# Optimization experiments

Measured on AMD Instinct MI355X. Metric: run time of the kernel, lower is better.

Reference implementation:

```python
import jax, jax.numpy as jnp
import numpy as np

POS_IDX = np.array([0, 2, 4, 10, 14, 20, 22, 24])   # +w taps on 5x5 ring
NEG_IDX = np.array([6, 7, 8, 11, 13, 16, 17, 18])   # -w taps on inner 3x3 ring (center stays 0)


def setup_inputs() -> dict:
    key = jax.random.key(0)
    kx, kw = jax.random.split(key)
    x = jax.random.normal(kx, (16, 256, 128, 128), dtype=jnp.float32)
    weight = jax.random.normal(kw, (256, 1, 3, 3), dtype=jnp.float32) * 0.1
    return {"x": x, "weight": weight}


def _build_rpdc_kernel(weight):
    # weight: [C, 1, 3, 3] -> sparse 5x5 kernel [C, 1, 5, 5]
    C = weight.shape[0]
    w = weight.reshape(C, 1, 9)
    tap = w[:, :, 1:]  # taps 1..8 (skip w[0]); center of 5x5 is forced to 0
    buf = jnp.zeros((C, 1, 25), dtype=weight.dtype)
    buf = buf.at[:, :, POS_IDX].set(tap)
    buf = buf.at[:, :, NEG_IDX].set(-tap)
    return buf.reshape(C, 1, 5, 5)


def reference(x, weight):
    # Depthwise conv (groups = in_channels), dilation=1 -> padding = 2 (same conv)
    C = weight.shape[0]
    kernel = _build_rpdc_kernel(weight)
    return jax.lax.conv_general_dilated(
        x, kernel,
        window_strides=(1, 1),
        padding=[(2, 2), (2, 2)],
        rhs_dilation=(1, 1),
        dimension_numbers=("NCHW", "OIHW", "NCHW"),
        feature_group_count=C,
    )
```

## Files before the change

### kernel.cpp

```cpp
#include <hip/hip_runtime.h>


#define HH 128
#define WW 128
#define CHUNK 32
#define SPB 8

__device__ __forceinline__ float bperm(int addr, float v) {
    return __int_as_float(__builtin_amdgcn_ds_bpermute(addr, __float_as_int(v)));
}

__global__ __launch_bounds__(256, 4) void rpdc_kernel(
    const float* __restrict__ x, const float* __restrict__ wt,
    float* __restrict__ out, int C)
{
    const int tid   = threadIdx.x;
    const int l     = tid & 31;
    const int s     = blockIdx.x * SPB + (tid >> 5);
    const int plane = s >> 2;
    const int h0    = (s & 3) * CHUNK;
    const int c     = plane & (C - 1);

    const float* wp = wt + (size_t)c * 9;
    const float t0 = wp[1], t1 = wp[2], t2 = wp[3], t3 = wp[4];
    const float t4 = wp[5], t5 = wp[6], t6 = wp[7], t7 = wp[8];

    const int w0 = l * 4;
    const float ml = (l == 0) ? 0.f : 1.f;
    const float mr = (l == 31) ? 0.f : 1.f;

    const int lane = tid & 63;
    const int upA  = ((lane - 1) & 63) * 4;
    const int dnA  = ((lane + 1) & 63) * 4;

    const float* xb = x + (size_t)plane * (HH * WW) + (size_t)h0 * WW + w0;
    float* ob = out + (size_t)plane * (HH * WW) + (size_t)h0 * WW + w0;

    float ring[6][8];
    float4 s0, s1;

    auto issue = [&](int rr, float4& v) {
        const int r = h0 + rr;
        if ((unsigned)r < (unsigned)HH) {
            v = *(const float4*)(xb + rr * WW);
        } else {
            v = make_float4(0.f, 0.f, 0.f, 0.f);
        }
    };
    auto insert = [&](float (&row)[8], const float4& v) {
        row[0] = bperm(upA, v.z) * ml;
        row[1] = bperm(upA, v.w) * ml;
        row[2] = v.x; row[3] = v.y; row[4] = v.z; row[5] = v.w;
        row[6] = bperm(dnA, v.x) * mr;
        row[7] = bperm(dnA, v.y) * mr;
    };

#pragma unroll
    for (int k = 0; k < 5; ++k) {
        float4 v;
        issue(k - 2, v);
        insert(ring[k], v);
    }
    issue(3, s0);
    issue(4, s1);

#pragma unroll
    for (int h = 0; h < CHUNK; ++h) {
        float4 nv;
        issue((h <= CHUNK - 4) ? (h + 5) : HH, nv);

        insert(ring[(h + 5) % 6], s0);
        s0 = s1; s1 = nv;

        const float (&A)[8]  = ring[h % 6];
        const float (&B)[8]  = ring[(h + 1) % 6];
        const float (&Cc)[8] = ring[(h + 2) % 6];
        const float (&D)[8]  = ring[(h + 3) % 6];
        const float (&E)[8]  = ring[(h + 4) % 6];

        float o[4];
#pragma unroll
        for (int j = 0; j < 4; ++j) {
            float r = t0 * (A[j]     - B[j + 1]);
            r      += t1 * (A[j + 2] - B[j + 2]);
            r      += t2 * (A[j + 4] - B[j + 3]);
            r      += t3 * (Cc[j]     - Cc[j + 1]);
            r      += t4 * (Cc[j + 4] - Cc[j + 3]);
            r      += t5 * (E[j]     - D[j + 1]);
            r      += t6 * (E[j + 2] - D[j + 2]);
            r      += t7 * (E[j + 4] - D[j + 3]);
            o[j] = r;
        }
        *(float4*)(ob + h * WW) = make_float4(o[0], o[1], o[2], o[3]);
    }
}

extern "C" void kernel_launch(void* const* d_in, const int* in_sizes, int n_in,
                              void* d_out, int out_size, void* d_ws, size_t ws_size,
                              hipStream_t stream) {
    const float* x = (const float*)d_in[0];
    const float* wt = (const float*)d_in[1];
    float* out = (float*)d_out;

    const int C = in_sizes[1] / 9;
    const int planes = in_sizes[0] / (HH * WW);

    dim3 grid(planes * (HH / CHUNK) / SPB);
    dim3 block(256);
    rpdc_kernel<<<grid, block, 0, stream>>>(x, wt, out, C);
}
```

Measured before the change: 436.8 us.

## Scatter input rows into rolling output accumulators instead of keeping a row ring

The stencil now works in scatter form. Each incoming row is halo-extended once and its contributions are added into a rolling set of five output accumulators, with a finished row written out as soon as it completes. This drops the six-row input ring of eight floats per row, cutting register pressure, and the launch-bounds hint is raised to ask for 8 waves-per-SIMD occupancy. The unrolled loop gains more conditional branches, and capping registers could force spills.

```diff
diff --git a/kernel.cpp b/kernel.cpp
--- a/kernel.cpp
+++ b/kernel.cpp
@@ -10,7 +10,7 @@
     return __int_as_float(__builtin_amdgcn_ds_bpermute(addr, __float_as_int(v)));
 }
 
-__global__ __launch_bounds__(256, 4) void rpdc_kernel(
+__global__ __launch_bounds__(256, 8) void rpdc_kernel(
     const float* __restrict__ x, const float* __restrict__ wt,
     float* __restrict__ out, int C)
 {
@@ -33,65 +33,73 @@
     const int upA  = ((lane - 1) & 63) * 4;
     const int dnA  = ((lane + 1) & 63) * 4;
 
-    const float* xb = x + (size_t)plane * (HH * WW) + (size_t)h0 * WW + w0;
-    float* ob = out + (size_t)plane * (HH * WW) + (size_t)h0 * WW + w0;
+    const float* pn = x + (size_t)plane * (HH * WW) + (size_t)(h0 - 2) * WW + w0;
+    int rn = h0 - 2;
+    float* po = out + (size_t)plane * (HH * WW) + (size_t)h0 * WW + w0;
 
-    float ring[6][8];
+    float acc[5][4];
     float4 s0, s1;
 
-    auto issue = [&](int rr, float4& v) {
-        const int r = h0 + rr;
-        if ((unsigned)r < (unsigned)HH) {
-            v = *(const float4*)(xb + rr * WW);
+    auto issue = [&](float4& v) {
+        if ((unsigned)rn < (unsigned)HH) {
+            v = *(const float4*)pn;
         } else {
             v = make_float4(0.f, 0.f, 0.f, 0.f);
         }
-    };
-    auto insert = [&](float (&row)[8], const float4& v) {
-        row[0] = bperm(upA, v.z) * ml;
-        row[1] = bperm(upA, v.w) * ml;
-        row[2] = v.x; row[3] = v.y; row[4] = v.z; row[5] = v.w;
-        row[6] = bperm(dnA, v.x) * mr;
-        row[7] = bperm(dnA, v.y) * mr;
+        pn += WW; ++rn;
     };
 
-#pragma unroll
-    for (int k = 0; k < 5; ++k) {
-        float4 v;
-        issue(k - 2, v);
-        insert(ring[k], v);
-    }
-    issue(3, s0);
-    issue(4, s1);
+    issue(s0);
+    issue(s1);
 
 #pragma unroll
-    for (int h = 0; h < CHUNK; ++h) {
+    for (int i = 0; i < CHUNK + 4; ++i) {
+        const int rr = i - 2;
+
         float4 nv;
-        issue((h <= CHUNK - 4) ? (h + 5) : HH, nv);
+        if (i < CHUNK + 2) issue(nv);
+        else nv = make_float4(0.f, 0.f, 0.f, 0.f);
 
-        insert(ring[(h + 5) % 6], s0);
+        float X[8];
+        X[0] = bperm(upA, s0.z) * ml;
+        X[1] = bperm(upA, s0.w) * ml;
+        X[2] = s0.x; X[3] = s0.y; X[4] = s0.z; X[5] = s0.w;
+        X[6] = bperm(dnA, s0.x) * mr;
+        X[7] = bperm(dnA, s0.y) * mr;
         s0 = s1; s1 = nv;
 
-        const float (&A)[8]  = ring[h % 6];
-        const float (&B)[8]  = ring[(h + 1) % 6];
-        const float (&Cc)[8] = ring[(h + 2) % 6];
-        const float (&D)[8]  = ring[(h + 3) % 6];
-        const float (&E)[8]  = ring[(h + 4) % 6];
-
-        float o[4];
+        if (rr + 2 < CHUNK) {
+            float* a = acc[(rr + 2) % 5];
 #pragma unroll
-        for (int j = 0; j < 4; ++j) {
-            float r = t0 * (A[j]     - B[j + 1]);
-            r      += t1 * (A[j + 2] - B[j + 2]);
-            r      += t2 * (A[j + 4] - B[j + 3]);
-            r      += t3 * (Cc[j]     - Cc[j + 1]);
-            r      += t4 * (Cc[j + 4] - Cc[j + 3]);
-            r      += t5 * (E[j]     - D[j + 1]);
-            r      += t6 * (E[j + 2] - D[j + 2]);
-            r      += t7 * (E[j + 4] - D[j + 3]);
-            o[j] = r;
+            for (int j = 0; j < 4; ++j)
+                a[j] = t0 * X[j] + t1 * X[j + 2] + t2 * X[j + 4];
         }
-        *(float4*)(ob + h * WW) = make_float4(o[0], o[1], o[2], o[3]);
+        if (rr + 1 >= 0 && rr + 1 < CHUNK) {
+            float* a = acc[(rr + 1) % 5];
+#pragma unroll
+            for (int j = 0; j < 4; ++j)
+                a[j] -= t0 * X[j + 1] + t1 * X[j + 2] + t2 * X[j + 3];
+        }
+        if (rr >= 0 && rr < CHUNK) {
+            float* a = acc[rr % 5];
+#pragma unroll
+            for (int j = 0; j < 4; ++j)
+                a[j] += t3 * (X[j] - X[j + 1]) + t4 * (X[j + 4] - X[j + 3]);
+        }
+        if (rr - 1 >= 0 && rr - 1 < CHUNK) {
+            float* a = acc[(rr - 1) % 5];
+#pragma unroll
+            for (int j = 0; j < 4; ++j)
+                a[j] -= t5 * X[j + 1] + t6 * X[j + 2] + t7 * X[j + 3];
+        }
+        if (rr - 2 >= 0) {
+            float* a = acc[(rr - 2) % 5];
+#pragma unroll
+            for (int j = 0; j < 4; ++j)
+                a[j] += t5 * X[j] + t6 * X[j + 2] + t7 * X[j + 4];
+            *(float4*)po = make_float4(a[0], a[1], a[2], a[3]);
+            po += WW;
+        }
     }
 }
 
```

Result: slower. 1.096 ms (+150.9%).

## Scatter each input row into five rolling accumulators instead of holding a row ring

Applied to the files above, without the earlier changes.

Replaces the 6-row register ring with a scatter formulation: each expanded input row is loaded once and immediately contributes to five in-flight output accumulators (float4 each), with the finished output stored when its last role completes. This cuts live registers from 48 ring floats to 20 accumulator floats plus 8 row floats, and launch bounds are raised to 8 waves per SIMD to increase occupancy. Weights are made wave-uniform with readfirstlane so they can live in scalar registers. Risk is that the heavier unroll or register pressure under the tighter bound could spill, and the reordered accumulation changes floating-point rounding slightly.

```diff
diff --git a/kernel.cpp b/kernel.cpp
--- a/kernel.cpp
+++ b/kernel.cpp
@@ -9,8 +9,53 @@
 __device__ __forceinline__ float bperm(int addr, float v) {
     return __int_as_float(__builtin_amdgcn_ds_bpermute(addr, __float_as_int(v)));
 }
+__device__ __forceinline__ float rfl(float v) {
+    return __int_as_float(__builtin_amdgcn_readfirstlane(__float_as_int(v)));
+}
 
-__global__ __launch_bounds__(256, 4) void rpdc_kernel(
+#define LOADROW(dst) { \
+    if ((unsigned)rn < (unsigned)HH) dst = *(const float4*)pn; \
+    else dst = make_float4(0.f, 0.f, 0.f, 0.f); \
+    pn += WW; ++rn; }
+
+#define EXT_SHIFT(DO_LOAD) { \
+    float4 nv_; \
+    if (DO_LOAD) { LOADROW(nv_) } \
+    else nv_ = make_float4(0.f, 0.f, 0.f, 0.f); \
+    x0 = bperm(upA, s0.z) * ml;  x1 = bperm(upA, s0.w) * ml; \
+    x2 = s0.x; x3 = s0.y; x4 = s0.z; x5 = s0.w; \
+    x6 = bperm(dnA, s0.x) * mr;  x7 = bperm(dnA, s0.y) * mr; \
+    s0 = s1; s1 = nv_; }
+
+#define ROLE_A(q) { \
+    q.x = t0*x0 + t1*x2 + t2*x4;  q.y = t0*x1 + t1*x3 + t2*x5; \
+    q.z = t0*x2 + t1*x4 + t2*x6;  q.w = t0*x3 + t1*x5 + t2*x7; }
+#define ROLE_B(q) { \
+    q.x -= t0*x1 + t1*x2 + t2*x3;  q.y -= t0*x2 + t1*x3 + t2*x4; \
+    q.z -= t0*x3 + t1*x4 + t2*x5;  q.w -= t0*x4 + t1*x5 + t2*x6; }
+#define ROLE_C(q) { \
+    q.x += t3*(x0-x1) + t4*(x4-x3);  q.y += t3*(x1-x2) + t4*(x5-x4); \
+    q.z += t3*(x2-x3) + t4*(x6-x5);  q.w += t3*(x3-x4) + t4*(x7-x6); }
+#define ROLE_D(q) { \
+    q.x -= t5*x1 + t6*x2 + t7*x3;  q.y -= t5*x2 + t6*x3 + t7*x4; \
+    q.z -= t5*x3 + t6*x4 + t7*x5;  q.w -= t5*x4 + t6*x5 + t7*x6; }
+#define ROLE_E(q) { \
+    q.x += t5*x0 + t6*x2 + t7*x4;  q.y += t5*x1 + t6*x3 + t7*x5; \
+    q.z += t5*x2 + t6*x4 + t7*x6;  q.w += t5*x3 + t6*x5 + t7*x7; \
+    *(float4*)po = q;  po += WW; }
+
+#define FULL(qA, qB, qC, qD, qE) { \
+    EXT_SHIFT(1) \
+    ROLE_A(qA) ROLE_B(qB) ROLE_C(qC) ROLE_D(qD) ROLE_E(qE) }
+
+#define CYCLE5() \
+    FULL(q4, q3, q2, q1, q0) \
+    FULL(q0, q4, q3, q2, q1) \
+    FULL(q1, q0, q4, q3, q2) \
+    FULL(q2, q1, q0, q4, q3) \
+    FULL(q3, q2, q1, q0, q4)
+
+__global__ __launch_bounds__(256, 8) void rpdc_kernel(
     const float* __restrict__ x, const float* __restrict__ wt,
     float* __restrict__ out, int C)
 {
@@ -22,77 +67,41 @@
     const int c     = plane & (C - 1);
 
     const float* wp = wt + (size_t)c * 9;
-    const float t0 = wp[1], t1 = wp[2], t2 = wp[3], t3 = wp[4];
-    const float t4 = wp[5], t5 = wp[6], t6 = wp[7], t7 = wp[8];
+    const float t0 = rfl(wp[1]), t1 = rfl(wp[2]), t2 = rfl(wp[3]), t3 = rfl(wp[4]);
+    const float t4 = rfl(wp[5]), t5 = rfl(wp[6]), t6 = rfl(wp[7]), t7 = rfl(wp[8]);
 
     const int w0 = l * 4;
     const float ml = (l == 0) ? 0.f : 1.f;
     const float mr = (l == 31) ? 0.f : 1.f;
-
     const int lane = tid & 63;
     const int upA  = ((lane - 1) & 63) * 4;
     const int dnA  = ((lane + 1) & 63) * 4;
 
-    const float* xb = x + (size_t)plane * (HH * WW) + (size_t)h0 * WW + w0;
-    float* ob = out + (size_t)plane * (HH * WW) + (size_t)h0 * WW + w0;
+    const float* pn = x + (size_t)plane * (HH * WW) + (ptrdiff_t)(h0 - 2) * WW + w0;
+    int rn = h0 - 2;
+    float* po = out + (size_t)plane * (HH * WW) + (size_t)h0 * WW + w0;
 
-    float ring[6][8];
+    float4 q0, q1, q2, q3, q4;
     float4 s0, s1;
+    float x0, x1, x2, x3, x4, x5, x6, x7;
 
-    auto issue = [&](int rr, float4& v) {
-        const int r = h0 + rr;
-        if ((unsigned)r < (unsigned)HH) {
-            v = *(const float4*)(xb + rr * WW);
-        } else {
-            v = make_float4(0.f, 0.f, 0.f, 0.f);
-        }
-    };
-    auto insert = [&](float (&row)[8], const float4& v) {
-        row[0] = bperm(upA, v.z) * ml;
-        row[1] = bperm(upA, v.w) * ml;
-        row[2] = v.x; row[3] = v.y; row[4] = v.z; row[5] = v.w;
-        row[6] = bperm(dnA, v.x) * mr;
-        row[7] = bperm(dnA, v.y) * mr;
-    };
+    LOADROW(s0)
+    LOADROW(s1)
 
-#pragma unroll
-    for (int k = 0; k < 5; ++k) {
-        float4 v;
-        issue(k - 2, v);
-        insert(ring[k], v);
-    }
-    issue(3, s0);
-    issue(4, s1);
+    EXT_SHIFT(1) ROLE_A(q0)
+    EXT_SHIFT(1) ROLE_A(q1) ROLE_B(q0)
+    EXT_SHIFT(1) ROLE_A(q2) ROLE_B(q1) ROLE_C(q0)
+    EXT_SHIFT(1) ROLE_A(q3) ROLE_B(q2) ROLE_C(q1) ROLE_D(q0)
 
-#pragma unroll
-    for (int h = 0; h < CHUNK; ++h) {
-        float4 nv;
-        issue((h <= CHUNK - 4) ? (h + 5) : HH, nv);
+    CYCLE5() CYCLE5() CYCLE5() CYCLE5() CYCLE5()
+    FULL(q4, q3, q2, q1, q0)
+    FULL(q0, q4, q3, q2, q1)
+    FULL(q1, q0, q4, q3, q2)
 
-        insert(ring[(h + 5) % 6], s0);
-        s0 = s1; s1 = nv;
-
-        const float (&A)[8]  = ring[h % 6];
-        const float (&B)[8]  = ring[(h + 1) % 6];
-        const float (&Cc)[8] = ring[(h + 2) % 6];
-        const float (&D)[8]  = ring[(h + 3) % 6];
-        const float (&E)[8]  = ring[(h + 4) % 6];
-
-        float o[4];
-#pragma unroll
-        for (int j = 0; j < 4; ++j) {
-            float r = t0 * (A[j]     - B[j + 1]);
-            r      += t1 * (A[j + 2] - B[j + 2]);
-            r      += t2 * (A[j + 4] - B[j + 3]);
-            r      += t3 * (Cc[j]     - Cc[j + 1]);
-            r      += t4 * (Cc[j + 4] - Cc[j + 3]);
-            r      += t5 * (E[j]     - D[j + 1]);
-            r      += t6 * (E[j + 2] - D[j + 2]);
-            r      += t7 * (E[j + 4] - D[j + 3]);
-            o[j] = r;
-        }
-        *(float4*)(ob + h * WW) = make_float4(o[0], o[1], o[2], o[3]);
-    }
+    EXT_SHIFT(1) ROLE_B(q1) ROLE_C(q0) ROLE_D(q4) ROLE_E(q3)
+    EXT_SHIFT(1) ROLE_C(q1) ROLE_D(q0) ROLE_E(q4)
+    EXT_SHIFT(0) ROLE_D(q1) ROLE_E(q0)
+    EXT_SHIFT(0) ROLE_E(q1)
 }
 
 extern "C" void kernel_launch(void* const* d_in, const int* in_sizes, int n_in,
```

After: 1.087 ms. 149% more time.
